# Performance work log

Measured on AMD Instinct MI355X. Metric: run time of the kernel, lower is better.

The kernel has to match this reference:

```python
import jax, jax.numpy as jnp
import numpy as np

THRESHOLD = 0.5
NEG_POS_RATIO = 3
ALPHA = 1.0
B, N_OBJ, N_PRIORS, N_CLASSES = 64, 32, 8732, 81


def xy_to_cxcy(xy):
    return jnp.concatenate([(xy[..., :2] + xy[..., 2:]) / 2.0, xy[..., 2:] - xy[..., :2]], axis=-1)


def cxcy_to_gcxgcy(cxcy, priors):
    return jnp.concatenate([
        (cxcy[..., :2] - priors[..., :2]) / (priors[..., 2:] / 10.0),
        jnp.log(cxcy[..., 2:] / priors[..., 2:]) * 5.0,
    ], axis=-1)


def jaccard(a, b):
    # a: [n,4], b: [m,4], both interpreted as (x1,y1,x2,y2) -- the original code
    # passes priors_cxcy directly (faithfully reproduced here).
    lt = jnp.maximum(a[:, None, :2], b[None, :, :2])
    rb = jnp.minimum(a[:, None, 2:], b[None, :, 2:])
    inter = jnp.prod(jnp.clip(rb - lt, 0.0, None), axis=-1)          # [n,m]
    area_a = jnp.prod(a[:, 2:] - a[:, :2], axis=-1)                  # [n]
    area_b = jnp.prod(b[:, 2:] - b[:, :2], axis=-1)                  # [m]
    return inter / (area_a[:, None] + area_b[None, :] - inter)


def _match(boxes_i, labels_i, priors_cxcy):
    # boxes_i: [n_obj,4] xy, labels_i: [n_obj] int, priors_cxcy: [n_priors,4]
    n_obj = boxes_i.shape[0]
    ov = jaccard(boxes_i, priors_cxcy)                               # [n_obj, n_priors]
    ov_for_prior = ov.max(axis=0)                                    # [n_priors]
    obj_for_prior = ov.argmax(axis=0)                                # [n_priors]
    prior_for_obj = ov.argmax(axis=1)                                # [n_obj]
    obj_for_prior = obj_for_prior.at[prior_for_obj].set(jnp.arange(n_obj))
    ov_for_prior = ov_for_prior.at[prior_for_obj].set(1.0)
    lab = labels_i[obj_for_prior]
    lab = jnp.where(ov_for_prior < THRESHOLD, 0, lab)                # background
    true_locs = cxcy_to_gcxgcy(xy_to_cxcy(boxes_i[obj_for_prior]), priors_cxcy)
    return true_locs, lab


def setup_inputs() -> dict:
    key = jax.random.key(0)
    k1, k2, k3, k4, k5, k6, k7 = jax.random.split(key, 7)
    predicted_locs = jax.random.normal(k1, (B, N_PRIORS, 4), dtype=jnp.float32)
    predicted_scores = jax.random.normal(k2, (B, N_PRIORS, N_CLASSES), dtype=jnp.float32)
    # valid gt boxes in xy form, inside [0,1]
    cxy = 0.15 + 0.7 * jax.random.uniform(k3, (B, N_OBJ, 2))
    wh = 0.05 + 0.25 * jax.random.uniform(k4, (B, N_OBJ, 2))
    boxes = jnp.clip(jnp.concatenate([cxy - wh / 2, cxy + wh / 2], axis=-1), 0.0, 1.0).astype(jnp.float32)
    labels = jax.random.randint(k5, (B, N_OBJ), 1, N_CLASSES)        # foreground classes
    # priors: cx,cy small, w,h large so that treating (cx,cy,w,h) as xy (as the
    # original code does in jaccard) still yields positive areas
    p_cxy = 0.4 * jax.random.uniform(k6, (N_PRIORS, 2))
    p_wh = 0.5 + 0.5 * jax.random.uniform(k7, (N_PRIORS, 2))
    priors_cxcy = jnp.concatenate([p_cxy, p_wh], axis=-1).astype(jnp.float32)
    return {
        "predicted_locs": predicted_locs,
        "predicted_scores": predicted_scores,
        "boxes": boxes,
        "labels": labels,
        "priors_cxcy": priors_cxcy,
    }


def multibox_loss(predicted_locs, predicted_scores, boxes, labels, priors_cxcy):
    n_priors = priors_cxcy.shape[0]
    true_locs, true_classes = jax.vmap(_match, in_axes=(0, 0, None))(boxes, labels, priors_cxcy)
    pos = true_classes != 0                                          # [B, n_priors]
    pos_f = pos.astype(predicted_locs.dtype)
    n_pos = pos.sum(axis=1)                                          # [B]
    n_pos_total = n_pos.sum().astype(jnp.float32)
    # nn.L1Loss(): mean over the 4 coords of positive priors
    loc_loss = (jnp.abs(predicted_locs - true_locs) * pos_f[..., None]).sum() / (n_pos_total * 4.0)
    # per-prior cross entropy
    logp = jax.nn.log_softmax(predicted_scores, axis=-1)             # [B,P,C]
    ce = -jnp.take_along_axis(logp, true_classes[..., None], axis=-1)[..., 0]  # [B,P]
    conf_pos = (ce * pos_f).sum()
    ce_neg = jnp.where(pos, 0.0, ce)
    ce_neg_sorted = -jnp.sort(-ce_neg, axis=1)                       # descending
    ranks = jnp.arange(n_priors)[None, :]
    hard = (ranks < (NEG_POS_RATIO * n_pos)[:, None]).astype(ce.dtype)
    conf_hard_neg = (ce_neg_sorted * hard).sum()
    conf_loss = (conf_hard_neg + conf_pos) / n_pos_total
    return conf_loss + ALPHA * loc_loss


def reference(predicted_locs, predicted_scores, boxes, labels, priors_cxcy):
    return multibox_loss(predicted_locs, predicted_scores, boxes, labels, priors_cxcy)
```

## Files before the change

kernel.cpp:

```cpp
#include <hip/hip_runtime.h>
#include <math.h>
#include <stdint.h>

#define BATCH 64
#define N_OBJ 32
#define NP 8732
#define NC 81
#define THRESH 0.5f
#define ROWS_PER_BLK 64


__global__ void k_zero(int* n_pos, float* scal) {
    int t = threadIdx.x;
    if (t < BATCH) n_pos[t] = 0;
    if (t == 0) { scal[0] = 0.f; scal[1] = 0.f; scal[2] = 0.f; }
}

__device__ __forceinline__ float iou_box_prior(float x1, float y1, float x2, float y2,
                                               float areaA, float4 pr, float areaB) {
    float iw = fminf(x2, pr.z) - fmaxf(x1, pr.x); iw = fmaxf(iw, 0.f);
    float ih = fminf(y2, pr.w) - fmaxf(y1, pr.y); ih = fmaxf(ih, 0.f);
    float inter = iw * ih;
    return inter / (areaA + areaB - inter);
}

__global__ void k_match_prior(const float* __restrict__ boxes,
                              const float* __restrict__ priors,
                              float* __restrict__ ovp, int* __restrict__ objp) {
    int i = blockIdx.y;
    __shared__ float bx[N_OBJ * 4];
    int t = threadIdx.x;
    if (t < N_OBJ * 4) bx[t] = boxes[i * N_OBJ * 4 + t];
    __syncthreads();
    int p = blockIdx.x * blockDim.x + t;
    if (p >= NP) return;
    float4 pr = ((const float4*)priors)[p];
    float areaB = (pr.z - pr.x) * (pr.w - pr.y);
    float best = -1.0f; int bestj = 0;
    for (int j = 0; j < N_OBJ; ++j) {
        float x1 = bx[j * 4 + 0], y1 = bx[j * 4 + 1], x2 = bx[j * 4 + 2], y2 = bx[j * 4 + 3];
        float areaA = (x2 - x1) * (y2 - y1);
        float v = iou_box_prior(x1, y1, x2, y2, areaA, pr, areaB);
        if (v > best) { best = v; bestj = j; }
    }
    ovp[i * NP + p] = best;
    objp[i * NP + p] = bestj;
}

__global__ void k_match_obj(const float* __restrict__ boxes,
                            const float* __restrict__ priors,
                            int* __restrict__ pfo) {
    int j = blockIdx.x, i = blockIdx.y;
    const float* bp = boxes + (i * N_OBJ + j) * 4;
    float x1 = bp[0], y1 = bp[1], x2 = bp[2], y2 = bp[3];
    float areaA = (x2 - x1) * (y2 - y1);
    float best = -1.f; int bestp = NP;
    for (int p = threadIdx.x; p < NP; p += blockDim.x) {
        float4 pr = ((const float4*)priors)[p];
        float areaB = (pr.z - pr.x) * (pr.w - pr.y);
        float v = iou_box_prior(x1, y1, x2, y2, areaA, pr, areaB);
        if (v > best) { best = v; bestp = p; }
    }
    __shared__ float sv[256];
    __shared__ int   si[256];
    int t = threadIdx.x;
    sv[t] = best; si[t] = bestp;
    __syncthreads();
    for (int s = 128; s > 0; s >>= 1) {
        if (t < s) {
            float v2 = sv[t + s]; int i2 = si[t + s];
            if (v2 > sv[t] || (v2 == sv[t] && i2 < si[t])) { sv[t] = v2; si[t] = i2; }
        }
        __syncthreads();
    }
    if (t == 0) pfo[i * N_OBJ + j] = si[0];
}

__global__ void k_force(const int* __restrict__ pfo,
                        float* __restrict__ ovp, int* __restrict__ objp) {
    int i = blockIdx.x * blockDim.x + threadIdx.x;
    if (i >= BATCH) return;
    for (int j = 0; j < N_OBJ; ++j) {
        int p = pfo[i * N_OBJ + j];
        objp[i * NP + p] = j;
        ovp[i * NP + p] = 1.0f;
    }
}

__global__ void __launch_bounds__(256)
k_ce(const float* __restrict__ scores,
     const float* __restrict__ plocs,
     const float* __restrict__ boxes,
     const int*   __restrict__ labels,
     const float* __restrict__ priors,
     const float* __restrict__ ovp,
     const int*   __restrict__ objp,
     float* __restrict__ ce_neg,
     int* __restrict__ n_pos, float* __restrict__ scal) {
    __shared__ float smem[ROWS_PER_BLK * NC];
    __shared__ float acc_cpos, acc_loc;
    __shared__ int   acc_np;
    int i  = blockIdx.y;
    int p0 = blockIdx.x * ROWS_PER_BLK;
    int rows = NP - p0; if (rows > ROWS_PER_BLK) rows = ROWS_PER_BLK;
    int t = threadIdx.x;
    if (t == 0) { acc_cpos = 0.f; acc_loc = 0.f; acc_np = 0; }

    const float* g = scores + ((size_t)i * NP + p0) * NC;
    int cnt = rows * NC;
    #pragma unroll 7
    for (int idx = t; idx < cnt; idx += 256) smem[idx] = g[idx];
    __syncthreads();

    int r = t >> 2, c = t & 3;
    bool active = (r < rows);
    float x[21];
    float m = -INFINITY;
    int nx = 0;
    if (active) {
        for (int e = c; e < NC; e += 4) { x[nx] = smem[r * NC + e]; m = fmaxf(m, x[nx]); ++nx; }
    }
    m = fmaxf(m, __shfl_xor(m, 1));
    m = fmaxf(m, __shfl_xor(m, 2));
    float s = 0.f;
    for (int q = 0; q < nx; ++q) s += __expf(x[q] - m);
    s += __shfl_xor(s, 1);
    s += __shfl_xor(s, 2);

    if (active && c == 0) {
        float lse = m + __logf(s);
        int gi = i * NP + p0 + r;
        int   obj = objp[gi];
        float ov  = ovp[gi];
        int   lab = (ov < THRESH) ? 0 : labels[i * N_OBJ + obj];
        float ce = lse - smem[r * NC + lab];
        if (lab != 0) {
            atomicAdd(&acc_np, 1);
            atomicAdd(&acc_cpos, ce);
            const float* bp = boxes + (i * N_OBJ + obj) * 4;
            float x1 = bp[0], y1 = bp[1], x2 = bp[2], y2 = bp[3];
            float bcx = (x1 + x2) * 0.5f, bcy = (y1 + y2) * 0.5f;
            float bw = x2 - x1, bh = y2 - y1;
            float4 pr = ((const float4*)priors)[p0 + r];
            float g0 = (bcx - pr.x) / (pr.z / 10.0f);
            float g1 = (bcy - pr.y) / (pr.w / 10.0f);
            float g2 = logf(bw / pr.z) * 5.0f;
            float g3 = logf(bh / pr.w) * 5.0f;
            const float* pl = plocs + (size_t)gi * 4;
            float l = fabsf(pl[0] - g0) + fabsf(pl[1] - g1)
                    + fabsf(pl[2] - g2) + fabsf(pl[3] - g3);
            atomicAdd(&acc_loc, l);
            ce_neg[gi] = 0.f;
        } else {
            ce_neg[gi] = ce;
        }
    }
    __syncthreads();
    if (t == 0 && acc_np > 0) {
        atomicAdd(&n_pos[i], acc_np);
        atomicAdd(&scal[0], acc_cpos);
        atomicAdd(&scal[2], acc_loc);
    }
}

__global__ void __launch_bounds__(256)
k_topk(const float* __restrict__ ce_neg,
       const int* __restrict__ n_pos, float* __restrict__ scal) {
    int i = blockIdx.x;
    int t = threadIdx.x;
    float x[35];
    #pragma unroll
    for (int j = 0; j < 35; ++j) {
        int p = t + j * 256;
        x[j] = (p < NP) ? ce_neg[i * NP + p] : 0.f;
    }
    int k = 3 * n_pos[i];
    if (k > NP) k = NP;
    if (k <= 0) return;

    __shared__ int   cnt_s[4];
    __shared__ float sum_s[4];
    unsigned lo = 0u, hi = 0x7F800001u;
    while (hi - lo > 1u) {
        unsigned mid = lo + ((hi - lo) >> 1);
        int c = 0;
        #pragma unroll
        for (int j = 0; j < 35; ++j) c += (__float_as_uint(x[j]) >= mid) ? 1 : 0;
        #pragma unroll
        for (int off = 32; off; off >>= 1) c += __shfl_xor(c, off);
        if ((t & 63) == 0) cnt_s[t >> 6] = c;
        __syncthreads();
        int total = cnt_s[0] + cnt_s[1] + cnt_s[2] + cnt_s[3];
        __syncthreads();
        if (total >= k) lo = mid; else hi = mid;
    }
    float vk = __uint_as_float(lo);

    float s = 0.f; int c = 0;
    #pragma unroll
    for (int j = 0; j < 35; ++j) {
        float v = x[j];
        if (v > vk) { s += v; c++; }
    }
    #pragma unroll
    for (int off = 32; off; off >>= 1) { s += __shfl_xor(s, off); c += __shfl_xor(c, off); }
    if ((t & 63) == 0) { sum_s[t >> 6] = s; cnt_s[t >> 6] = c; }
    __syncthreads();
    if (t == 0) {
        float st = sum_s[0] + sum_s[1] + sum_s[2] + sum_s[3];
        int   ct = cnt_s[0] + cnt_s[1] + cnt_s[2] + cnt_s[3];
        atomicAdd(&scal[1], st + (float)(k - ct) * vk);
    }
}

__global__ void k_final(const int* __restrict__ n_pos,
                        const float* __restrict__ scal, float* __restrict__ out) {
    if (threadIdx.x == 0) {
        int nt = 0;
        for (int i = 0; i < BATCH; ++i) nt += n_pos[i];
        float nf = (float)nt;
        out[0] = (scal[1] + scal[0]) / nf + scal[2] / (nf * 4.0f);
    }
}

extern "C" void kernel_launch(void* const* d_in, const int* in_sizes, int n_in,
                              void* d_out, int out_size, void* d_ws, size_t ws_size,
                              hipStream_t stream) {
    const float* plocs  = (const float*)d_in[0];
    const float* scores = (const float*)d_in[1];
    const float* boxes  = (const float*)d_in[2];
    const int*   labels = (const int*)d_in[3];
    const float* priors = (const float*)d_in[4];
    float* out = (float*)d_out;

    char* ws = (char*)d_ws;
    size_t bp = (size_t)BATCH * NP * 4;
    float* ovp    = (float*)(ws);
    int*   objp   = (int*)  (ws + bp);
    float* ce_neg = (float*)(ws + 2 * bp);
    int*   pfo    = (int*)  (ws + 3 * bp);
    int*   n_pos  = pfo + BATCH * N_OBJ;
    float* scal   = (float*)(n_pos + BATCH);

    hipLaunchKernelGGL(k_zero, dim3(1), dim3(64), 0, stream, n_pos, scal);
    hipLaunchKernelGGL(k_match_prior, dim3((NP + 255) / 256, BATCH), dim3(256), 0, stream,
                       boxes, priors, ovp, objp);
    hipLaunchKernelGGL(k_match_obj, dim3(N_OBJ, BATCH), dim3(256), 0, stream,
                       boxes, priors, pfo);
    hipLaunchKernelGGL(k_force, dim3(1), dim3(64), 0, stream, pfo, ovp, objp);
    hipLaunchKernelGGL(k_ce, dim3((NP + ROWS_PER_BLK - 1) / ROWS_PER_BLK, BATCH), dim3(256), 0, stream,
                       scores, plocs, boxes, labels, priors, ovp, objp, ce_neg, n_pos, scal);
    hipLaunchKernelGGL(k_topk, dim3(BATCH), dim3(256), 0, stream, ce_neg, n_pos, scal);
    hipLaunchKernelGGL(k_final, dim3(1), dim3(1), 0, stream, n_pos, scal, out);
}
```

Measured before the change: 199.3 us.

## Vectorize score loads to shared memory, fold zero-init kernel, unroll IoU loop

```diff
diff --git a/kernel.cpp b/kernel.cpp
--- a/kernel.cpp
+++ b/kernel.cpp
@@ -10,12 +10,6 @@
 #define ROWS_PER_BLK 64
 
 
-__global__ void k_zero(int* n_pos, float* scal) {
-    int t = threadIdx.x;
-    if (t < BATCH) n_pos[t] = 0;
-    if (t == 0) { scal[0] = 0.f; scal[1] = 0.f; scal[2] = 0.f; }
-}
-
 __device__ __forceinline__ float iou_box_prior(float x1, float y1, float x2, float y2,
                                                float areaA, float4 pr, float areaB) {
     float iw = fminf(x2, pr.z) - fmaxf(x1, pr.x); iw = fmaxf(iw, 0.f);
@@ -26,10 +20,15 @@
 
 __global__ void k_match_prior(const float* __restrict__ boxes,
                               const float* __restrict__ priors,
-                              float* __restrict__ ovp, int* __restrict__ objp) {
+                              float* __restrict__ ovp, int* __restrict__ objp,
+                              int* __restrict__ n_pos, float* __restrict__ scal) {
     int i = blockIdx.y;
+    int t = threadIdx.x;
+    if (blockIdx.x == 0 && i == 0) {
+        if (t < BATCH) n_pos[t] = 0;
+        if (t < 3) scal[t] = 0.f;
+    }
     __shared__ float bx[N_OBJ * 4];
-    int t = threadIdx.x;
     if (t < N_OBJ * 4) bx[t] = boxes[i * N_OBJ * 4 + t];
     __syncthreads();
     int p = blockIdx.x * blockDim.x + t;
@@ -37,6 +36,7 @@
     float4 pr = ((const float4*)priors)[p];
     float areaB = (pr.z - pr.x) * (pr.w - pr.y);
     float best = -1.0f; int bestj = 0;
+    #pragma unroll
     for (int j = 0; j < N_OBJ; ++j) {
         float x1 = bx[j * 4 + 0], y1 = bx[j * 4 + 1], x2 = bx[j * 4 + 2], y2 = bx[j * 4 + 3];
         float areaA = (x2 - x1) * (y2 - y1);
@@ -97,7 +97,7 @@
      const int*   __restrict__ objp,
      float* __restrict__ ce_neg,
      int* __restrict__ n_pos, float* __restrict__ scal) {
-    __shared__ float smem[ROWS_PER_BLK * NC];
+    __shared__ __align__(16) float smem[ROWS_PER_BLK * NC];
     __shared__ float acc_cpos, acc_loc;
     __shared__ int   acc_np;
     int i  = blockIdx.y;
@@ -106,24 +106,26 @@
     int t = threadIdx.x;
     if (t == 0) { acc_cpos = 0.f; acc_loc = 0.f; acc_np = 0; }
 
-    const float* g = scores + ((size_t)i * NP + p0) * NC;
-    int cnt = rows * NC;
-    #pragma unroll 7
-    for (int idx = t; idx < cnt; idx += 256) smem[idx] = g[idx];
+    const float4* g4 = (const float4*)(scores + ((size_t)i * NP + p0) * NC);
+    float4* s4 = (float4*)smem;
+    int cnt4 = (rows * NC) >> 2;
+    for (int idx = t; idx < cnt4; idx += 256) s4[idx] = g4[idx];
     __syncthreads();
 
     int r = t >> 2, c = t & 3;
     bool active = (r < rows);
-    float x[21];
+    const float* row = smem + r * NC;
+
     float m = -INFINITY;
-    int nx = 0;
     if (active) {
-        for (int e = c; e < NC; e += 4) { x[nx] = smem[r * NC + e]; m = fmaxf(m, x[nx]); ++nx; }
+        for (int e = c; e < NC; e += 4) m = fmaxf(m, row[e]);
     }
     m = fmaxf(m, __shfl_xor(m, 1));
     m = fmaxf(m, __shfl_xor(m, 2));
     float s = 0.f;
-    for (int q = 0; q < nx; ++q) s += __expf(x[q] - m);
+    if (active) {
+        for (int e = c; e < NC; e += 4) s += __expf(row[e] - m);
+    }
     s += __shfl_xor(s, 1);
     s += __shfl_xor(s, 2);
 
@@ -133,7 +135,7 @@
         int   obj = objp[gi];
         float ov  = ovp[gi];
         int   lab = (ov < THRESH) ? 0 : labels[i * N_OBJ + obj];
-        float ce = lse - smem[r * NC + lab];
+        float ce = lse - row[lab];
         if (lab != 0) {
             atomicAdd(&acc_np, 1);
             atomicAdd(&acc_cpos, ce);
@@ -242,9 +244,8 @@
     int*   n_pos  = pfo + BATCH * N_OBJ;
     float* scal   = (float*)(n_pos + BATCH);
 
-    hipLaunchKernelGGL(k_zero, dim3(1), dim3(64), 0, stream, n_pos, scal);
     hipLaunchKernelGGL(k_match_prior, dim3((NP + 255) / 256, BATCH), dim3(256), 0, stream,
-                       boxes, priors, ovp, objp);
+                       boxes, priors, ovp, objp, n_pos, scal);
     hipLaunchKernelGGL(k_match_obj, dim3(N_OBJ, BATCH), dim3(256), 0, stream,
                        boxes, priors, pfo);
     hipLaunchKernelGGL(k_force, dim3(1), dim3(64), 0, stream, pfo, ovp, objp);
```

Result: faster. 191.7 us (-3.8%).
